# Kernel tuning notes

Measured on AMD Instinct MI355X. Metric: run time of the kernel, lower is better.

Reference implementation:

```python
import jax, jax.numpy as jnp
import numpy as np

PH = PW = 7          # pooled output size
SR = 2               # sampling_ratio: SR x SR samples per bin
SCALES = (0.25, 0.125, 0.0625, 0.03125)  # FPN strides 4,8,16,32
K = 512              # number of ROIs
B = 2                # batch (images)
IMG = 800.0


def _coords(start, bsize, P):
    # sample coords for P bins, SR samples per bin: start + p*bin + (i+0.5)*bin/SR
    j = jnp.arange(P * SR, dtype=start.dtype)
    return (start[:, None]
            + (j // SR)[None, :] * bsize[:, None]
            + ((j % SR) + 0.5)[None, :] * (bsize[:, None] / SR))  # [K, P*SR]


def _roi_align_level(feat, rois, scale):
    # feat: [B, C, H, W] ; rois: [K, 5] (batch_idx, x1, y1, x2, y2 in image coords)
    Bf, C, H, W = feat.shape
    b = rois[:, 0].astype(jnp.int32)
    x1 = rois[:, 1] * scale
    y1 = rois[:, 2] * scale
    x2 = rois[:, 3] * scale
    y2 = rois[:, 4] * scale
    roi_w = jnp.maximum(x2 - x1, 1.0)   # legacy (aligned=False) ROIAlign
    roi_h = jnp.maximum(y2 - y1, 1.0)
    ys = _coords(y1, roi_h / PH, PH)    # [K, Sy]
    xs = _coords(x1, roi_w / PW, PW)    # [K, Sx]
    y = ys[:, :, None]                  # [K, Sy, 1]
    x = xs[:, None, :]                  # [K, 1, Sx]
    valid = (y > -1.0) & (y < H) & (x > -1.0) & (x < W)  # [K, Sy, Sx]
    yc = jnp.clip(y, 0.0, None)
    xc = jnp.clip(x, 0.0, None)
    yl = jnp.minimum(yc.astype(jnp.int32), H - 1)
    xl = jnp.minimum(xc.astype(jnp.int32), W - 1)
    yh = jnp.minimum(yl + 1, H - 1)
    xh = jnp.minimum(xl + 1, W - 1)
    ly = jnp.where(yl >= H - 1, 0.0, yc - yl)
    lx = jnp.where(xl >= W - 1, 0.0, xc - xl)
    hy, hx = 1.0 - ly, 1.0 - lx
    feat_flat = feat.reshape(Bf, C, H * W)
    Sy, Sx = PH * SR, PW * SR
    acc = jnp.zeros((rois.shape[0], C, Sy, Sx), feat.dtype)
    corners = ((yl, xl, hy * hx), (yl, xh, hy * lx),
               (yh, xl, ly * hx), (yh, xh, ly * lx))
    for yy, xx, w in corners:  # fixed 4-corner loop (not a data-dim loop)
        idx = jnp.broadcast_to(yy * W + xx, (rois.shape[0], Sy, Sx))
        vals = jax.vmap(lambda bi, ii: jnp.take(feat_flat, bi, axis=0)[:, ii])(b, idx)
        acc = acc + vals * jnp.broadcast_to(w, idx.shape)[:, None, :, :]
    acc = jnp.where(valid[:, None, :, :], acc, 0.0)
    # average SRxSR samples within each 7x7 bin
    return acc.reshape(rois.shape[0], C, PH, SR, PW, SR).mean(axis=(3, 5))


def setup_inputs() -> dict:
    key = jax.random.key(0)
    ks = jax.random.split(key, 10)
    input_0 = jax.random.normal(ks[0], (B, 256, 200, 200), jnp.float32)
    input_1 = jax.random.normal(ks[1], (B, 256, 100, 100), jnp.float32)
    input_2 = jax.random.normal(ks[2], (B, 256, 50, 50), jnp.float32)
    input_3 = jax.random.normal(ks[3], (B, 256, 25, 25), jnp.float32)
    bidx = jax.random.randint(ks[4], (K,), 0, B).astype(jnp.float32)
    x1 = jax.random.uniform(ks[5], (K,)) * (IMG - 64.0)
    y1 = jax.random.uniform(ks[6], (K,)) * (IMG - 64.0)
    bw = 32.0 + jax.random.uniform(ks[7], (K,)) * 200.0
    bh = 32.0 + jax.random.uniform(ks[8], (K,)) * 200.0
    rois = jnp.stack([bidx, x1, y1,
                      jnp.minimum(x1 + bw, IMG),
                      jnp.minimum(y1 + bh, IMG)], axis=1).astype(jnp.float32)
    level = jax.random.randint(ks[9], (K,), 0, 4).astype(jnp.int32)
    rois_counts = jnp.array([K // 2, K - K // 2], jnp.int32)  # unused (all ROIs valid)
    return {"input_0": input_0, "input_1": input_1, "input_2": input_2,
            "input_3": input_3, "rois": rois, "rois_counts": rois_counts,
            "level": level}


def reference(input_0, input_1, input_2, input_3, rois, rois_counts, level):
    feats = (input_0, input_1, input_2, input_3)
    lvl = level.astype(jnp.int32)
    out = jnp.zeros((rois.shape[0], input_0.shape[1], PH, PW), input_0.dtype)
    for i, (f, s) in enumerate(zip(feats, SCALES)):
        o = _roi_align_level(f, rois, s)
        out = out + jnp.where((lvl == i)[:, None, None, None], o, 0.0)
    return out
```

## Files before the change

kernel.cpp:

```cpp
#include <hip/hip_runtime.h>


#define NUM_CH 256
#define CPT    4
#define CGRP   64
#define WPR    49
#define PAIRS  3136

typedef float floatx2 __attribute__((ext_vector_type(2)));
typedef float floatx4 __attribute__((ext_vector_type(4)));

__device__ __forceinline__ float ext4(floatx4 v, int i) {
    float r = (i == 1) ? v.y : v.x;
    r = (i == 2) ? v.z : r;
    r = (i == 3) ? v.w : r;
    return r;
}

__global__ __launch_bounds__(256) void roi_align_kernel(
    const float* __restrict__ f0,
    const float* __restrict__ f1,
    const float* __restrict__ f2,
    const float* __restrict__ f3,
    const float* __restrict__ rois_f,
    const int* __restrict__ level,
    float* __restrict__ out,
    int K,
    int NW)
{
    int nb  = gridDim.x;
    int q   = nb >> 3, r = nb & 7;
    int xcd = blockIdx.x & 7;
    int idx = blockIdx.x >> 3;
    int l   = xcd * q + min(xcd, r) + idx;

    int wid = l * 4 + (int)(threadIdx.x >> 6);
    if (wid >= NW) return;
    int lane = threadIdx.x & 63;

    int k = wid % K;
    int g = wid / K;
    k = __builtin_amdgcn_readfirstlane(k);
    g = __builtin_amdgcn_readfirstlane(g);

    int pair = g * 64 + lane;
    int c2   = pair / 49;
    int p    = pair - c2 * 49;
    int ph = p / 7;
    int pw = p % 7;

    int lvl = level[k];
    const float* f;
    int H, W; float scale;
    if (lvl == 0)      { f = f0; H = 200; W = 200; scale = 0.25f;    }
    else if (lvl == 1) { f = f1; H = 100; W = 100; scale = 0.125f;   }
    else if (lvl == 2) { f = f2; H = 50;  W = 50;  scale = 0.0625f;  }
    else               { f = f3; H = 25;  W = 25;  scale = 0.03125f; }

    const float* rf = rois_f + (size_t)k * 5;
    float r0 = rf[0];
    float x1 = rf[1] * scale, y1 = rf[2] * scale;
    float x2 = rf[3] * scale, y2 = rf[4] * scale;
    int bi = (int)r0;
    bi = (bi < 0) ? 0 : ((bi > 1) ? 1 : bi);

    float bh = fmaxf(y2 - y1, 1.0f) * (1.0f / 7.0f);
    float bw = fmaxf(x2 - x1, 1.0f) * (1.0f / 7.0f);

    const size_t plane = (size_t)(H * W);
    const float* base  = f + ((size_t)bi * NUM_CH + c2) * plane;
    const size_t cstr  = (size_t)CGRP * plane;

    int   rA[2], rB[2];
    float lyv[2], hyv[2], vy[2];
    #pragma unroll
    for (int sy = 0; sy < 2; ++sy) {
        float y = y1 + (float)ph * bh + ((float)sy + 0.5f) * (bh * 0.5f);
        bool valid = (y > -1.0f) && (y < (float)H);
        float yc = fmaxf(y, 0.0f);
        int yl = min((int)yc, H - 1);
        int yh = min(yl + 1, H - 1);
        float ly = (yl >= H - 1) ? 0.0f : (yc - (float)yl);
        rA[sy] = yl * W;
        rB[sy] = yh * W;
        lyv[sy] = ly; hyv[sy] = 1.0f - ly;
        vy[sy] = valid ? 0.25f : 0.0f;
    }
    int   xlv[2], xhv[2];
    float lxv[2], hxv[2], vx[2];
    #pragma unroll
    for (int sx = 0; sx < 2; ++sx) {
        float x = x1 + (float)pw * bw + ((float)sx + 0.5f) * (bw * 0.5f);
        bool valid = (x > -1.0f) && (x < (float)W);
        float xc = fmaxf(x, 0.0f);
        int xl = min((int)xc, W - 1);
        float lx = (xl >= W - 1) ? 0.0f : (xc - (float)xl);
        xlv[sx] = xl;
        xhv[sx] = min(xl + 1, W - 1);
        lxv[sx] = lx; hxv[sx] = 1.0f - lx;
        vx[sx] = valid ? 1.0f : 0.0f;
    }

    bool same = (rA[1] == rA[0]);

    float acc[CPT];
    #pragma unroll
    for (int j = 0; j < CPT; ++j) acc[j] = 0.0f;

    if (bw <= 3.98f) {
        int xq = min(xlv[0], W - 4);
        int i0l = min(max(xlv[0] - xq, 0), 3);
        int i0h = min(max(xhv[0] - xq, 0), 3);
        int i1l = min(max(xlv[1] - xq, 0), 3);
        int i1h = min(max(xhv[1] - xq, 0), 3);

        floatx4 LA[CPT], LB[CPT];
        #pragma unroll
        for (int j = 0; j < CPT; ++j) {
            const float* bj = base + (size_t)j * cstr;
            LA[j] = *(const floatx4*)(bj + rA[0] + xq);
            LB[j] = *(const floatx4*)(bj + rB[0] + xq);
        }
        #pragma unroll
        for (int sy = 0; sy < 2; ++sy) {
            if (sy == 1 && !same) {
                #pragma unroll
                for (int j = 0; j < CPT; ++j) {
                    const float* bj = base + (size_t)j * cstr;
                    LA[j] = *(const floatx4*)(bj + rA[1] + xq);
                    LB[j] = *(const floatx4*)(bj + rB[1] + xq);
                }
            }
            #pragma unroll
            for (int sx = 0; sx < 2; ++sx) {
                int il = sx ? i1l : i0l;
                int ih = sx ? i1h : i0h;
                float vs  = vy[sy] * vx[sx];
                float w00 = hyv[sy] * hxv[sx] * vs;
                float w01 = hyv[sy] * lxv[sx] * vs;
                float w10 = lyv[sy] * hxv[sx] * vs;
                float w11 = lyv[sy] * lxv[sx] * vs;
                #pragma unroll
                for (int j = 0; j < CPT; ++j) {
                    acc[j] += w00 * ext4(LA[j], il) + w01 * ext4(LA[j], ih)
                            + w10 * ext4(LB[j], il) + w11 * ext4(LB[j], ih);
                }
            }
        }
    } else {
        int   xb[2];
        float sel[2];
        #pragma unroll
        for (int sx = 0; sx < 2; ++sx) {
            int xq = min(xlv[sx], W - 2);
            xb[sx]  = xq;
            sel[sx] = (xlv[sx] > xq) ? 1.0f : 0.0f;
        }
        floatx2 va[CPT][2], vb[CPT][2];
        #pragma unroll
        for (int sx = 0; sx < 2; ++sx) {
            #pragma unroll
            for (int j = 0; j < CPT; ++j) {
                const float* bj = base + (size_t)j * cstr;
                va[j][sx] = *(const floatx2*)(bj + rA[0] + xb[sx]);
                vb[j][sx] = *(const floatx2*)(bj + rB[0] + xb[sx]);
            }
        }
        #pragma unroll
        for (int sy = 0; sy < 2; ++sy) {
            if (sy == 1 && !same) {
                #pragma unroll
                for (int sx = 0; sx < 2; ++sx) {
                    #pragma unroll
                    for (int j = 0; j < CPT; ++j) {
                        const float* bj = base + (size_t)j * cstr;
                        va[j][sx] = *(const floatx2*)(bj + rA[1] + xb[sx]);
                        vb[j][sx] = *(const floatx2*)(bj + rB[1] + xb[sx]);
                    }
                }
            }
            #pragma unroll
            for (int sx = 0; sx < 2; ++sx) {
                float vs  = vy[sy] * vx[sx];
                float w00 = hyv[sy] * hxv[sx] * vs;
                float w01 = hyv[sy] * lxv[sx] * vs;
                float w10 = lyv[sy] * hxv[sx] * vs;
                float w11 = lyv[sy] * lxv[sx] * vs;
                float s0  = sel[sx];
                #pragma unroll
                for (int j = 0; j < CPT; ++j) {
                    float v00 = va[j][sx].x + s0 * (va[j][sx].y - va[j][sx].x);
                    float v10 = vb[j][sx].x + s0 * (vb[j][sx].y - vb[j][sx].x);
                    acc[j] += w00 * v00 + w01 * va[j][sx].y
                            + w10 * v10 + w11 * vb[j][sx].y;
                }
            }
        }
    }

    size_t ob = (size_t)k * (NUM_CH * 49) + (size_t)g * 64 + lane;
    #pragma unroll
    for (int j = 0; j < CPT; ++j)
        out[ob + (size_t)j * PAIRS] = acc[j];
}

extern "C" void kernel_launch(void* const* d_in, const int* in_sizes, int n_in,
                              void* d_out, int out_size, void* d_ws, size_t ws_size,
                              hipStream_t stream) {
    const float* f0   = (const float*)d_in[0];
    const float* f1   = (const float*)d_in[1];
    const float* f2   = (const float*)d_in[2];
    const float* f3   = (const float*)d_in[3];
    const float* rois = (const float*)d_in[4];
    const int* level = (const int*)d_in[6];
    float* out = (float*)d_out;

    int K  = out_size / (NUM_CH * 49);
    int NW = K * WPR;
    int threads = 256;
    int blocks  = (NW + 3) / 4;
    roi_align_kernel<<<blocks, threads, 0, stream>>>(f0, f1, f2, f3, rois, level, out, K, NW);
}
```

Measured before the change: 185.9 us.

## Stage coarse-level ROI patches in LDS, keep direct gather for level 0

Splits the grid into two block types. Level-0 ROIs keep the original per-wavefront direct global gather. ROIs on levels 1-3 get new blocks that cooperatively copy the ROI's feature patch for chunks of channels into shared memory and then do bilinear sampling from LDS. This aims to cut redundant global loads for small coarse-level patches. In exchange it adds many early-exit blocks, uses only 245 of 256 threads for compute, adds barriers, and requests 32KB of dynamic LDS per block, which may lower occupancy for the level-0 path too.

```diff
diff --git a/kernel.cpp b/kernel.cpp
--- a/kernel.cpp
+++ b/kernel.cpp
@@ -1,11 +1,9 @@
 #include <hip/hip_runtime.h>
 
 
-#define NUM_CH 256
-#define CPT    4
-#define CGRP   64
-#define WPR    49
-#define PAIRS  3136
+#define NUM_CH    256
+#define WPR       49
+#define LDS_BYTES 32768
 
 typedef float floatx2 __attribute__((ext_vector_type(2)));
 typedef float floatx4 __attribute__((ext_vector_type(4)));
@@ -26,182 +24,296 @@
     const int* __restrict__ level,
     float* __restrict__ out,
     int K,
-    int NW)
+    int GBLK)
 {
-    int nb  = gridDim.x;
-    int q   = nb >> 3, r = nb & 7;
-    int xcd = blockIdx.x & 7;
-    int idx = blockIdx.x >> 3;
-    int l   = xcd * q + min(xcd, r) + idx;
-
-    int wid = l * 4 + (int)(threadIdx.x >> 6);
-    if (wid >= NW) return;
-    int lane = threadIdx.x & 63;
-
-    int k = wid % K;
-    int g = wid / K;
-    k = __builtin_amdgcn_readfirstlane(k);
-    g = __builtin_amdgcn_readfirstlane(g);
-
-    int pair = g * 64 + lane;
-    int c2   = pair / 49;
-    int p    = pair - c2 * 49;
-    int ph = p / 7;
-    int pw = p % 7;
-
-    int lvl = level[k];
-    const float* f;
-    int H, W; float scale;
-    if (lvl == 0)      { f = f0; H = 200; W = 200; scale = 0.25f;    }
-    else if (lvl == 1) { f = f1; H = 100; W = 100; scale = 0.125f;   }
-    else if (lvl == 2) { f = f2; H = 50;  W = 50;  scale = 0.0625f;  }
-    else               { f = f3; H = 25;  W = 25;  scale = 0.03125f; }
-
-    const float* rf = rois_f + (size_t)k * 5;
-    float r0 = rf[0];
-    float x1 = rf[1] * scale, y1 = rf[2] * scale;
-    float x2 = rf[3] * scale, y2 = rf[4] * scale;
-    int bi = (int)r0;
-    bi = (bi < 0) ? 0 : ((bi > 1) ? 1 : bi);
-
-    float bh = fmaxf(y2 - y1, 1.0f) * (1.0f / 7.0f);
-    float bw = fmaxf(x2 - x1, 1.0f) * (1.0f / 7.0f);
-
-    const size_t plane = (size_t)(H * W);
-    const float* base  = f + ((size_t)bi * NUM_CH + c2) * plane;
-    const size_t cstr  = (size_t)CGRP * plane;
-
-    int   rA[2], rB[2];
-    float lyv[2], hyv[2], vy[2];
-    #pragma unroll
-    for (int sy = 0; sy < 2; ++sy) {
-        float y = y1 + (float)ph * bh + ((float)sy + 0.5f) * (bh * 0.5f);
-        bool valid = (y > -1.0f) && (y < (float)H);
-        float yc = fmaxf(y, 0.0f);
-        int yl = min((int)yc, H - 1);
-        int yh = min(yl + 1, H - 1);
-        float ly = (yl >= H - 1) ? 0.0f : (yc - (float)yl);
-        rA[sy] = yl * W;
-        rB[sy] = yh * W;
-        lyv[sy] = ly; hyv[sy] = 1.0f - ly;
-        vy[sy] = valid ? 0.25f : 0.0f;
+    extern __shared__ float smem[];
+
+    if ((int)blockIdx.x >= GBLK) {
+        int b = blockIdx.x - GBLK;
+        int k = b >> 2;
+        int q = b & 3;
+        int lvl = level[k];
+        if (lvl == 0) return;
+
+        const float* f; int H, W; float scale;
+        if (lvl == 1)      { f = f1; H = 100; W = 100; scale = 0.125f;   }
+        else if (lvl == 2) { f = f2; H = 50;  W = 50;  scale = 0.0625f;  }
+        else               { f = f3; H = 25;  W = 25;  scale = 0.03125f; }
+
+        const float* rf = rois_f + (size_t)k * 5;
+        float r0 = rf[0];
+        float x1 = rf[1] * scale, y1 = rf[2] * scale;
+        float x2 = rf[3] * scale, y2 = rf[4] * scale;
+        int bi = (int)r0;
+        bi = (bi < 0) ? 0 : ((bi > 1) ? 1 : bi);
+
+        float bh = fmaxf(y2 - y1, 1.0f) * (1.0f / 7.0f);
+        float bw = fmaxf(x2 - x1, 1.0f) * (1.0f / 7.0f);
+
+        float syn = y1 + 0.25f * bh, syx = y1 + 6.75f * bh;
+        int y0  = min((int)fmaxf(syn, 0.0f), H - 1);
+        int ylx = min((int)fmaxf(syx, 0.0f), H - 1);
+        int yhx = min(ylx + 1, H - 1);
+        int R   = yhx - y0 + 1;
+        float sxn = x1 + 0.25f * bw, sxx = x1 + 6.75f * bw;
+        int x0  = min((int)fmaxf(sxn, 0.0f), W - 1);
+        int xlx = min((int)fmaxf(sxx, 0.0f), W - 1);
+        int xhx = min(xlx + 1, W - 1);
+        int XC  = xhx - x0 + 1;
+
+        int patch = R * XC;
+        int C = (LDS_BYTES / 4) / patch;
+        C = min(C, 64); C = max(C, 1);
+
+        int tid = threadIdx.x;
+        int px  = tid % 49;
+        int cR  = tid / 49;
+        int ph = px / 7, pw = px % 7;
+
+        int ra[2], rb[2]; float lyv[2], hyv[2], vyv[2];
+        #pragma unroll
+        for (int sy = 0; sy < 2; ++sy) {
+            float y = y1 + (float)ph * bh + ((float)sy + 0.5f) * (bh * 0.5f);
+            bool valid = (y > -1.0f) && (y < (float)H);
+            float yc = fmaxf(y, 0.0f);
+            int yl = min((int)yc, H - 1);
+            int yh = min(yl + 1, H - 1);
+            float ly = (yl >= H - 1) ? 0.0f : (yc - (float)yl);
+            ra[sy] = (yl - y0) * XC;
+            rb[sy] = (yh - y0) * XC;
+            lyv[sy] = ly; hyv[sy] = 1.0f - ly;
+            vyv[sy] = valid ? 0.25f : 0.0f;
+        }
+        int xa[2], xb[2]; float lxv[2], hxv[2], vxv[2];
+        #pragma unroll
+        for (int sx = 0; sx < 2; ++sx) {
+            float x = x1 + (float)pw * bw + ((float)sx + 0.5f) * (bw * 0.5f);
+            bool valid = (x > -1.0f) && (x < (float)W);
+            float xc = fmaxf(x, 0.0f);
+            int xl = min((int)xc, W - 1);
+            float lx = (xl >= W - 1) ? 0.0f : (xc - (float)xl);
+            xa[sx] = xl - x0;
+            xb[sx] = min(xl + 1, W - 1) - x0;
+            lxv[sx] = lx; hxv[sx] = 1.0f - lx;
+            vxv[sx] = valid ? 1.0f : 0.0f;
+        }
+
+        const size_t plane = (size_t)(H * W);
+        const float* basec = f + ((size_t)bi * NUM_CH + q * 64) * plane;
+        size_t outb = (size_t)k * (NUM_CH * 49) + (size_t)(q * 64) * 49 + px;
+
+        for (int c0 = 0; c0 < 64; c0 += C) {
+            int Cc = min(C, 64 - c0);
+            int slots = Cc * patch;
+            for (int s = tid; s < slots; s += 256) {
+                int c   = s / patch;
+                int rem = s - c * patch;
+                int r   = rem / XC;
+                int x   = rem - r * XC;
+                smem[s] = basec[(size_t)(c0 + c) * plane
+                                + (size_t)((y0 + r) * W + x0 + x)];
+            }
+            __syncthreads();
+            if (cR < 5) {
+                for (int cc = cR; cc < Cc; cc += 5) {
+                    const float* P = smem + cc * patch;
+                    float acc = 0.0f;
+                    #pragma unroll
+                    for (int sy = 0; sy < 2; ++sy) {
+                        #pragma unroll
+                        for (int sx = 0; sx < 2; ++sx) {
+                            float v00 = P[ra[sy] + xa[sx]];
+                            float v01 = P[ra[sy] + xb[sx]];
+                            float v10 = P[rb[sy] + xa[sx]];
+                            float v11 = P[rb[sy] + xb[sx]];
+                            float vs  = vyv[sy] * vxv[sx];
+                            acc += vs * (hyv[sy] * (hxv[sx] * v00 + lxv[sx] * v01)
+                                       + lyv[sy] * (hxv[sx] * v10 + lxv[sx] * v11));
+                        }
+                    }
+                    out[outb + (size_t)(c0 + cc) * 49] = acc;
+                }
+            }
+            __syncthreads();
+        }
+        return;
     }
-    int   xlv[2], xhv[2];
-    float lxv[2], hxv[2], vx[2];
-    #pragma unroll
-    for (int sx = 0; sx < 2; ++sx) {
-        float x = x1 + (float)pw * bw + ((float)sx + 0.5f) * (bw * 0.5f);
-        bool valid = (x > -1.0f) && (x < (float)W);
-        float xc = fmaxf(x, 0.0f);
-        int xl = min((int)xc, W - 1);
-        float lx = (xl >= W - 1) ? 0.0f : (xc - (float)xl);
-        xlv[sx] = xl;
-        xhv[sx] = min(xl + 1, W - 1);
-        lxv[sx] = lx; hxv[sx] = 1.0f - lx;
-        vx[sx] = valid ? 1.0f : 0.0f;
-    }
-
-    bool same = (rA[1] == rA[0]);
-
-    float acc[CPT];
-    #pragma unroll
-    for (int j = 0; j < CPT; ++j) acc[j] = 0.0f;
-
-    if (bw <= 3.98f) {
-        int xq = min(xlv[0], W - 4);
-        int i0l = min(max(xlv[0] - xq, 0), 3);
-        int i0h = min(max(xhv[0] - xq, 0), 3);
-        int i1l = min(max(xlv[1] - xq, 0), 3);
-        int i1h = min(max(xhv[1] - xq, 0), 3);
-
-        floatx4 LA[CPT], LB[CPT];
-        #pragma unroll
-        for (int j = 0; j < CPT; ++j) {
-            const float* bj = base + (size_t)j * cstr;
-            LA[j] = *(const floatx4*)(bj + rA[0] + xq);
-            LB[j] = *(const floatx4*)(bj + rB[0] + xq);
-        }
+
+    {
+        int nb  = GBLK;
+        int q   = nb >> 3, r = nb & 7;
+        int xcd = blockIdx.x & 7;
+        int idx = blockIdx.x >> 3;
+        int l   = xcd * q + min(xcd, r) + idx;
+
+        int NW  = K * WPR;
+        int wid = l * 4 + (int)(threadIdx.x >> 6);
+        if (wid >= NW) return;
+        int lane = threadIdx.x & 63;
+
+        int k = wid % K;
+        int g = wid / K;
+        k = __builtin_amdgcn_readfirstlane(k);
+        g = __builtin_amdgcn_readfirstlane(g);
+
+        if (level[k] != 0) return;
+
+        const int H = 200, W = 200;
+        const float scale = 0.25f;
+        const float* f = f0;
+
+        int pair = g * 64 + lane;
+        int c2   = pair / 49;
+        int p    = pair - c2 * 49;
+        int ph = p / 7;
+        int pw = p % 7;
+
+        const float* rf = rois_f + (size_t)k * 5;
+        float r0 = rf[0];
+        float x1 = rf[1] * scale, y1 = rf[2] * scale;
+        float x2 = rf[3] * scale, y2 = rf[4] * scale;
+        int bi = (int)r0;
+        bi = (bi < 0) ? 0 : ((bi > 1) ? 1 : bi);
+
+        float bh = fmaxf(y2 - y1, 1.0f) * (1.0f / 7.0f);
+        float bw = fmaxf(x2 - x1, 1.0f) * (1.0f / 7.0f);
+
+        const size_t plane = (size_t)(H * W);
+        const float* base  = f + ((size_t)bi * NUM_CH + c2) * plane;
+        const size_t cstr  = (size_t)64 * plane;
+
+        int   rA[2], rB[2];
+        float lyv[2], hyv[2], vy[2];
         #pragma unroll
         for (int sy = 0; sy < 2; ++sy) {
-            if (sy == 1 && !same) {
-                #pragma unroll
-                for (int j = 0; j < CPT; ++j) {
-                    const float* bj = base + (size_t)j * cstr;
-                    LA[j] = *(const floatx4*)(bj + rA[1] + xq);
-                    LB[j] = *(const floatx4*)(bj + rB[1] + xq);
-                }
-            }
-            #pragma unroll
-            for (int sx = 0; sx < 2; ++sx) {
-                int il = sx ? i1l : i0l;
-                int ih = sx ? i1h : i0h;
-                float vs  = vy[sy] * vx[sx];
-                float w00 = hyv[sy] * hxv[sx] * vs;
-                float w01 = hyv[sy] * lxv[sx] * vs;
-                float w10 = lyv[sy] * hxv[sx] * vs;
-                float w11 = lyv[sy] * lxv[sx] * vs;
-                #pragma unroll
-                for (int j = 0; j < CPT; ++j) {
-                    acc[j] += w00 * ext4(LA[j], il) + w01 * ext4(LA[j], ih)
-                            + w10 * ext4(LB[j], il) + w11 * ext4(LB[j], ih);
-                }
-            }
-        }
-    } else {
-        int   xb[2];
-        float sel[2];
+            float y = y1 + (float)ph * bh + ((float)sy + 0.5f) * (bh * 0.5f);
+            bool valid = (y > -1.0f) && (y < (float)H);
+            float yc = fmaxf(y, 0.0f);
+            int yl = min((int)yc, H - 1);
+            int yh = min(yl + 1, H - 1);
+            float ly = (yl >= H - 1) ? 0.0f : (yc - (float)yl);
+            rA[sy] = yl * W;
+            rB[sy] = yh * W;
+            lyv[sy] = ly; hyv[sy] = 1.0f - ly;
+            vy[sy] = valid ? 0.25f : 0.0f;
+        }
+        int   xlv[2], xhv[2];
+        float lxv[2], hxv[2], vx[2];
         #pragma unroll
         for (int sx = 0; sx < 2; ++sx) {
-            int xq = min(xlv[sx], W - 2);
-            xb[sx]  = xq;
-            sel[sx] = (xlv[sx] > xq) ? 1.0f : 0.0f;
-        }
-        floatx2 va[CPT][2], vb[CPT][2];
-        #pragma unroll
-        for (int sx = 0; sx < 2; ++sx) {
-            #pragma unroll
-            for (int j = 0; j < CPT; ++j) {
+            float x = x1 + (float)pw * bw + ((float)sx + 0.5f) * (bw * 0.5f);
+            bool valid = (x > -1.0f) && (x < (float)W);
+            float xc = fmaxf(x, 0.0f);
+            int xl = min((int)xc, W - 1);
+            float lx = (xl >= W - 1) ? 0.0f : (xc - (float)xl);
+            xlv[sx] = xl;
+            xhv[sx] = min(xl + 1, W - 1);
+            lxv[sx] = lx; hxv[sx] = 1.0f - lx;
+            vx[sx] = valid ? 1.0f : 0.0f;
+        }
+
+        bool same = (rA[1] == rA[0]);
+
+        float acc[4];
+        #pragma unroll
+        for (int j = 0; j < 4; ++j) acc[j] = 0.0f;
+
+        if (bw <= 3.98f) {
+            int xq = min(xlv[0], W - 4);
+            int i0l = min(max(xlv[0] - xq, 0), 3);
+            int i0h = min(max(xhv[0] - xq, 0), 3);
+            int i1l = min(max(xlv[1] - xq, 0), 3);
+            int i1h = min(max(xhv[1] - xq, 0), 3);
+
+            floatx4 LA[4], LB[4];
+            #pragma unroll
+            for (int j = 0; j < 4; ++j) {
                 const float* bj = base + (size_t)j * cstr;
-                va[j][sx] = *(const floatx2*)(bj + rA[0] + xb[sx]);
-                vb[j][sx] = *(const floatx2*)(bj + rB[0] + xb[sx]);
-            }
-        }
-        #pragma unroll
-        for (int sy = 0; sy < 2; ++sy) {
-            if (sy == 1 && !same) {
+                LA[j] = *(const floatx4*)(bj + rA[0] + xq);
+                LB[j] = *(const floatx4*)(bj + rB[0] + xq);
+            }
+            #pragma unroll
+            for (int sy = 0; sy < 2; ++sy) {
+                if (sy == 1 && !same) {
+                    #pragma unroll
+                    for (int j = 0; j < 4; ++j) {
+                        const float* bj = base + (size_t)j * cstr;
+                        LA[j] = *(const floatx4*)(bj + rA[1] + xq);
+                        LB[j] = *(const floatx4*)(bj + rB[1] + xq);
+                    }
+                }
                 #pragma unroll
                 for (int sx = 0; sx < 2; ++sx) {
-                    #pragma unroll
-                    for (int j = 0; j < CPT; ++j) {
-                        const float* bj = base + (size_t)j * cstr;
-                        va[j][sx] = *(const floatx2*)(bj + rA[1] + xb[sx]);
-                        vb[j][sx] = *(const floatx2*)(bj + rB[1] + xb[sx]);
-                    }
-                }
-            }
+                    int il = sx ? i1l : i0l;
+                    int ih = sx ? i1h : i0h;
+                    float vs  = vy[sy] * vx[sx];
+                    float w00 = hyv[sy] * hxv[sx] * vs;
+                    float w01 = hyv[sy] * lxv[sx] * vs;
+                    float w10 = lyv[sy] * hxv[sx] * vs;
+                    float w11 = lyv[sy] * lxv[sx] * vs;
+                    #pragma unroll
+                    for (int j = 0; j < 4; ++j) {
+                        acc[j] += w00 * ext4(LA[j], il) + w01 * ext4(LA[j], ih)
+                                + w10 * ext4(LB[j], il) + w11 * ext4(LB[j], ih);
+                    }
+                }
+            }
+        } else {
+            int   xbq[2];
+            float sel[2];
             #pragma unroll
             for (int sx = 0; sx < 2; ++sx) {
-                float vs  = vy[sy] * vx[sx];
-                float w00 = hyv[sy] * hxv[sx] * vs;
-                float w01 = hyv[sy] * lxv[sx] * vs;
-                float w10 = lyv[sy] * hxv[sx] * vs;
-                float w11 = lyv[sy] * lxv[sx] * vs;
-                float s0  = sel[sx];
+                int xq = min(xlv[sx], W - 2);
+                xbq[sx] = xq;
+                sel[sx] = (xlv[sx] > xq) ? 1.0f : 0.0f;
+            }
+            floatx2 va[4][2], vb[4][2];
+            #pragma unroll
+            for (int sx = 0; sx < 2; ++sx) {
                 #pragma unroll
-                for (int j = 0; j < CPT; ++j) {
-                    float v00 = va[j][sx].x + s0 * (va[j][sx].y - va[j][sx].x);
-                    float v10 = vb[j][sx].x + s0 * (vb[j][sx].y - vb[j][sx].x);
-                    acc[j] += w00 * v00 + w01 * va[j][sx].y
-                            + w10 * v10 + w11 * vb[j][sx].y;
-                }
-            }
-        }
+                for (int j = 0; j < 4; ++j) {
+                    const float* bj = base + (size_t)j * cstr;
+                    va[j][sx] = *(const floatx2*)(bj + rA[0] + xbq[sx]);
+                    vb[j][sx] = *(const floatx2*)(bj + rB[0] + xbq[sx]);
+                }
+            }
+            #pragma unroll
+            for (int sy = 0; sy < 2; ++sy) {
+                if (sy == 1 && !same) {
+                    #pragma unroll
+                    for (int sx = 0; sx < 2; ++sx) {
+                        #pragma unroll
+                        for (int j = 0; j < 4; ++j) {
+                            const float* bj = base + (size_t)j * cstr;
+                            va[j][sx] = *(const floatx2*)(bj + rA[1] + xbq[sx]);
+                            vb[j][sx] = *(const floatx2*)(bj + rB[1] + xbq[sx]);
+                        }
+                    }
+                }
+                #pragma unroll
+                for (int sx = 0; sx < 2; ++sx) {
+                    float vs  = vy[sy] * vx[sx];
+                    float w00 = hyv[sy] * hxv[sx] * vs;
+                    float w01 = hyv[sy] * lxv[sx] * vs;
+                    float w10 = lyv[sy] * hxv[sx] * vs;
+                    float w11 = lyv[sy] * lxv[sx] * vs;
+                    float s0  = sel[sx];
+                    #pragma unroll
+                    for (int j = 0; j < 4; ++j) {
+                        float v00 = va[j][sx].x + s0 * (va[j][sx].y - va[j][sx].x);
+                        float v10 = vb[j][sx].x + s0 * (vb[j][sx].y - vb[j][sx].x);
+                        acc[j] += w00 * v00 + w01 * va[j][sx].y
+                                + w10 * v10 + w11 * vb[j][sx].y;
+                    }
+                }
+            }
+        }
+
+        size_t ob = (size_t)k * (NUM_CH * 49) + (size_t)g * 64 + lane;
+        #pragma unroll
+        for (int j = 0; j < 4; ++j)
+            out[ob + (size_t)j * 3136] = acc[j];
     }
-
-    size_t ob = (size_t)k * (NUM_CH * 49) + (size_t)g * 64 + lane;
-    #pragma unroll
-    for (int j = 0; j < CPT; ++j)
-        out[ob + (size_t)j * PAIRS] = acc[j];
 }
 
 extern "C" void kernel_launch(void* const* d_in, const int* in_sizes, int n_in,
@@ -215,9 +327,10 @@
     const int* level = (const int*)d_in[6];
     float* out = (float*)d_out;
 
-    int K  = out_size / (NUM_CH * 49);
-    int NW = K * WPR;
-    int threads = 256;
-    int blocks  = (NW + 3) / 4;
-    roi_align_kernel<<<blocks, threads, 0, stream>>>(f0, f1, f2, f3, rois, level, out, K, NW);
+    int K    = out_size / (NUM_CH * 49);
+    int GBLK = (K * WPR + 3) / 4;
+    int SBLK = K * 4;
+    int blocks = GBLK + SBLK;
+    roi_align_kernel<<<blocks, 256, LDS_BYTES, stream>>>(
+        f0, f1, f2, f3, rois, level, out, K, GBLK);
 }
```

Result: slower. 237.2 us (+27.6%).
